# Kernel optimization log

Measured on AMD Instinct MI355X. Metric: run time of the kernel, lower is better.

Reference implementation:

```python
import jax, jax.numpy as jnp
import numpy as np

B, C, Q, E = 32, 1024, 64, 256  # batch, max_context_len, max_question_len, embedding_size
FE = 4 * E                      # final_encoding_size (self_attention=False)


def setup_inputs() -> dict:
    key = jax.random.key(0)
    ks = jax.random.split(key, 7)
    return {
        "context": jax.random.normal(ks[0], (B, C, E), dtype=jnp.float32),
        "question": jax.random.normal(ks[1], (B, Q, E), dtype=jnp.float32),
        "context_mask": jnp.ones((B, C), dtype=jnp.float32),
        "w_question": jax.random.normal(ks[2], (E,), dtype=jnp.float32),
        "w_context": jax.random.normal(ks[3], (E,), dtype=jnp.float32),
        "w_multiple": jax.random.normal(ks[4], (E,), dtype=jnp.float32),
        "final_W": jax.random.normal(ks[5], (FE, FE), dtype=jnp.float32) * (1.0 / np.sqrt(FE)),
        "final_b": jnp.zeros((FE,), dtype=jnp.float32),
    }


def reference(context, question, context_mask, w_question, w_context, w_multiple, final_W, final_b):
    # Trilinear similarity: s[b,c,q] = <w_q, q_q> + <w_c, c_c> + <w_m, c_c * q_q>
    q_weighted = question @ w_question                 # (B, Q)
    ctx_weighted = context @ w_context                 # (B, C)
    # (question.unsqueeze(1) * context.unsqueeze(2)) @ w_multiple, computed
    # without materializing the (B, C, Q, E) intermediate:
    mult = jnp.einsum('bce,bqe->bcq', context * w_multiple, question)  # (B, C, Q)
    similarity = ctx_weighted[:, :, None] + q_weighted[:, None, :] + mult  # (B, C, Q)

    # Context-to-query attention (softmax over question dim)
    c2q_att = jnp.einsum('bcq,bqe->bce', jax.nn.softmax(similarity, axis=2), question)

    # Query-to-context attention (softmax over context dim of row-max scores)
    q2c_weights = jax.nn.softmax(jnp.max(similarity, axis=2), axis=1)   # (B, C)
    q2c_att = jnp.einsum('bc,bce->be', q2c_weights, context)            # (B, E)

    attended = jnp.concatenate(
        [context, c2q_att, context * c2q_att, context * q2c_att[:, None, :]],
        axis=2)                                                          # (B, C, 4E)

    # MaskedLinear: affine map, output rows zeroed where context_mask == 0
    out = (attended @ final_W.T + final_b) * context_mask[:, :, None]    # (B, C, 4E)
    return out
```

## Files before the change

### kernel.cpp

```cpp
#include <hip/hip_runtime.h>

#define BB 32
#define CC 1024
#define QQ 64
#define EE 256
#define FE 1024
#define MM (BB*CC)

typedef __bf16 bf16_t;
typedef bf16_t bf16x8 __attribute__((ext_vector_type(8)));
typedef float f32x4 __attribute__((ext_vector_type(4)));

__device__ __forceinline__ unsigned short f2bf(float f) {
  unsigned u = __float_as_uint(f);
  u += 0x7fffu + ((u >> 16) & 1u);
  return (unsigned short)(u >> 16);
}
__device__ __forceinline__ float bf2f(unsigned short u) {
  return __uint_as_float(((unsigned)u) << 16);
}

__device__ __forceinline__ void gload_lds16(const void* g, void* l) {
  __builtin_amdgcn_global_load_lds(
      (const __attribute__((address_space(1))) unsigned int*)g,
      (__attribute__((address_space(3))) unsigned int*)l, 16, 0, 0);
}

__global__ void k_prep(const float* __restrict__ question, const float* __restrict__ w_question,
                       const float* __restrict__ w_multiple, float* __restrict__ qm,
                       float* __restrict__ qw,
                       const float* __restrict__ W, unsigned short* __restrict__ Wb) {
  int bx = blockIdx.x;
  if (bx < 512) {
    int gid = bx * 256 + threadIdx.x;
    int row = gid >> 6;
    int lane = gid & 63;
    const float4 q = *(const float4*)(question + (size_t)row * EE + lane * 4);
    const float4 wm = *(const float4*)(w_multiple + lane * 4);
    const float4 wq = *(const float4*)(w_question + lane * 4);
    float4 r; r.x = q.x*wm.x; r.y = q.y*wm.y; r.z = q.z*wm.z; r.w = q.w*wm.w;
    *(float4*)(qm + (size_t)row * EE + lane * 4) = r;
    float d = q.x*wq.x + q.y*wq.y + q.z*wq.z + q.w*wq.w;
    d += __shfl_xor(d, 1);  d += __shfl_xor(d, 2);  d += __shfl_xor(d, 4);
    d += __shfl_xor(d, 8);  d += __shfl_xor(d, 16); d += __shfl_xor(d, 32);
    if (lane == 0) qw[row] = d;
  } else {
    int i = ((bx - 512) * 256 + threadIdx.x) * 4;
    float4 v = *(const float4*)(W + i);
    ushort4 o; o.x = f2bf(v.x); o.y = f2bf(v.y); o.z = f2bf(v.z); o.w = f2bf(v.w);
    *(ushort4*)(Wb + i) = o;
  }
}

#define DOT4(acc, A, Bv) acc += A.x*Bv.x + A.y*Bv.y + A.z*Bv.z + A.w*Bv.w

__launch_bounds__(256)
__global__ void k_sim(const float* __restrict__ ctx, const float* __restrict__ qm,
                      const float* __restrict__ qw_g, const float* __restrict__ w_context,
                      float* __restrict__ P, float* __restrict__ rowmax,
                      unsigned short* __restrict__ att) {
  __shared__ float qml[QQ][260];
  __shared__ float ck[64][36];
  __shared__ float cwl[64];
  __shared__ float qwl[QQ];
  const int tid = threadIdx.x;
  const int b = blockIdx.y;
  const int c0 = blockIdx.x * 64;
  const int tx = tid & 15, ty = tid >> 4;

  const float* qmb = qm + (size_t)b * (QQ * EE);
  for (int idx = tid * 4; idx < QQ * EE; idx += 1024) {
    float4 v = *(const float4*)(qmb + idx);
    *(float4*)&qml[idx >> 8][idx & 255] = v;
  }
  if (tid < QQ) qwl[tid] = qw_g[b * QQ + tid];

  const int cr = tid >> 3, er = (tid & 7) * 4;
  const float* crow0 = ctx + ((size_t)(b * CC + c0 + cr)) * EE;
  const float* crow1 = crow0 + 32 * EE;
  unsigned short* arow0 = att + ((size_t)(b * CC + c0 + cr)) * FE;
  unsigned short* arow1 = arow0 + (size_t)32 * FE;
  float s[4][4] = {{0.f}};
  float cp0 = 0.f, cp1 = 0.f;

  for (int eo = 0; eo < EE; eo += 32) {
    float4 cv0 = *(const float4*)(crow0 + eo + er);
    float4 cv1 = *(const float4*)(crow1 + eo + er);
    float4 wc = *(const float4*)(w_context + eo + er);
    cp0 += cv0.x*wc.x + cv0.y*wc.y + cv0.z*wc.z + cv0.w*wc.w;
    cp1 += cv1.x*wc.x + cv1.y*wc.y + cv1.z*wc.z + cv1.w*wc.w;
    ushort4 u0, u1;
    u0.x = f2bf(cv0.x); u0.y = f2bf(cv0.y); u0.z = f2bf(cv0.z); u0.w = f2bf(cv0.w);
    u1.x = f2bf(cv1.x); u1.y = f2bf(cv1.y); u1.z = f2bf(cv1.z); u1.w = f2bf(cv1.w);
    *(ushort4*)(arow0 + eo + er) = u0;
    *(ushort4*)(arow1 + eo + er) = u1;
    __syncthreads();
    *(float4*)&ck[cr][er] = cv0;
    *(float4*)&ck[cr + 32][er] = cv1;
    __syncthreads();
#pragma unroll
    for (int ee = 0; ee < 32; ee += 4) {
      float4 a0 = *(const float4*)&ck[ty +  0][ee];
      float4 a1 = *(const float4*)&ck[ty + 16][ee];
      float4 a2 = *(const float4*)&ck[ty + 32][ee];
      float4 a3 = *(const float4*)&ck[ty + 48][ee];
      float4 b0 = *(const float4*)&qml[tx +  0][eo + ee];
      float4 b1 = *(const float4*)&qml[tx + 16][eo + ee];
      float4 b2 = *(const float4*)&qml[tx + 32][eo + ee];
      float4 b3 = *(const float4*)&qml[tx + 48][eo + ee];
      DOT4(s[0][0], a0, b0); DOT4(s[0][1], a0, b1); DOT4(s[0][2], a0, b2); DOT4(s[0][3], a0, b3);
      DOT4(s[1][0], a1, b0); DOT4(s[1][1], a1, b1); DOT4(s[1][2], a1, b2); DOT4(s[1][3], a1, b3);
      DOT4(s[2][0], a2, b0); DOT4(s[2][1], a2, b1); DOT4(s[2][2], a2, b2); DOT4(s[2][3], a2, b3);
      DOT4(s[3][0], a3, b0); DOT4(s[3][1], a3, b1); DOT4(s[3][2], a3, b2); DOT4(s[3][3], a3, b3);
    }
  }
  cp0 += __shfl_xor(cp0, 1); cp0 += __shfl_xor(cp0, 2); cp0 += __shfl_xor(cp0, 4);
  cp1 += __shfl_xor(cp1, 1); cp1 += __shfl_xor(cp1, 2); cp1 += __shfl_xor(cp1, 4);
  if ((tid & 7) == 0) { cwl[cr] = cp0; cwl[cr + 32] = cp1; }
  __syncthreads();

#pragma unroll
  for (int i = 0; i < 4; ++i) {
    int c = ty + 16 * i;
    float cw = cwl[c];
    float f[4], mx = -1e30f;
#pragma unroll
    for (int j = 0; j < 4; ++j) {
      f[j] = s[i][j] + cw + qwl[tx + 16 * j];
      mx = fmaxf(mx, f[j]);
    }
    mx = fmaxf(mx, __shfl_xor(mx, 1));
    mx = fmaxf(mx, __shfl_xor(mx, 2));
    mx = fmaxf(mx, __shfl_xor(mx, 4));
    mx = fmaxf(mx, __shfl_xor(mx, 8));
    float sum = 0.f;
#pragma unroll
    for (int j = 0; j < 4; ++j) { f[j] = expf(f[j] - mx); sum += f[j]; }
    sum += __shfl_xor(sum, 1);
    sum += __shfl_xor(sum, 2);
    sum += __shfl_xor(sum, 4);
    sum += __shfl_xor(sum, 8);
    float inv = 1.f / sum;
    if (tx == 0) rowmax[(size_t)b * CC + c0 + c] = mx;
    size_t prow = ((size_t)(b * CC + c0 + c)) * QQ;
#pragma unroll
    for (int j = 0; j < 4; ++j) P[prow + tx + 16 * j] = f[j] * inv;
  }
}

__global__ void k_q2c_softmax(const float* __restrict__ rowmax, float* __restrict__ q2cw) {
  int b = blockIdx.x, tid = threadIdx.x;
  __shared__ float rbuf[4], sbuf[4];
  float4 v = *(const float4*)(rowmax + (size_t)b * CC + tid * 4);
  float m = fmaxf(fmaxf(v.x, v.y), fmaxf(v.z, v.w));
  for (int off = 1; off < 64; off <<= 1) m = fmaxf(m, __shfl_xor(m, off));
  int wv = tid >> 6;
  if ((tid & 63) == 0) rbuf[wv] = m;
  __syncthreads();
  m = fmaxf(fmaxf(rbuf[0], rbuf[1]), fmaxf(rbuf[2], rbuf[3]));
  float e0 = expf(v.x - m), e1 = expf(v.y - m), e2 = expf(v.z - m), e3 = expf(v.w - m);
  float sum = e0 + e1 + e2 + e3;
  for (int off = 1; off < 64; off <<= 1) sum += __shfl_xor(sum, off);
  if ((tid & 63) == 0) sbuf[wv] = sum;
  __syncthreads();
  sum = sbuf[0] + sbuf[1] + sbuf[2] + sbuf[3];
  float inv = 1.f / sum;
  float4 o; o.x = e0 * inv; o.y = e1 * inv; o.z = e2 * inv; o.w = e3 * inv;
  *(float4*)(q2cw + (size_t)b * CC + tid * 4) = o;
}

__global__ void k_q2c_part(const unsigned short* __restrict__ att, const float* __restrict__ w,
                           float* __restrict__ part) {
  int b = blockIdx.y, ch = blockIdx.x;
  int e = threadIdx.x;
  const unsigned short* base = att + ((size_t)(b * CC + ch * 128)) * FE + e;
  const float* wp = w + b * CC + ch * 128;
  float acc = 0.f;
#pragma unroll 4
  for (int c = 0; c < 128; ++c) acc += wp[c] * bf2f(base[(size_t)c * FE]);
  part[(b * 8 + ch) * EE + e] = acc;
}

__global__ void k_q2c_sum(const float* __restrict__ part, float* __restrict__ q2catt) {
  int b = blockIdx.x, e = threadIdx.x;
  float a = 0.f;
#pragma unroll
  for (int ch = 0; ch < 8; ++ch) a += part[(b * 8 + ch) * EE + e];
  q2catt[b * EE + e] = a;
}

__launch_bounds__(256)
__global__ void k_pv(const float* __restrict__ P, const float* __restrict__ question,
                     const float* __restrict__ q2catt, unsigned short* __restrict__ attended) {
  __shared__ float PT[QQ][65];
  __shared__ float ql[QQ][68];
  const int tid = threadIdx.x;
  const int b = blockIdx.y, c0 = blockIdx.x * 64;
  const int tx = tid & 15, ty = tid >> 4;

  {
    int q4 = (tid & 15) * 4, cb = tid >> 4;
#pragma unroll
    for (int r = 0; r < 4; ++r) {
      int c = cb + 16 * r;
      float4 v = *(const float4*)(P + ((size_t)(b * CC + c0 + c)) * QQ + q4);
      PT[q4 + 0][c] = v.x; PT[q4 + 1][c] = v.y; PT[q4 + 2][c] = v.z; PT[q4 + 3][c] = v.w;
    }
  }
  const float* qb = question + (size_t)b * (QQ * EE);
  const float* g2 = q2catt + b * EE;

  for (int ep = 0; ep < EE; ep += 64) {
    __syncthreads();
    {
      int q = tid >> 2, e16 = (tid & 3) * 16;
      const float* src = qb + (size_t)q * EE + ep + e16;
      float4 v0 = *(const float4*)(src);
      float4 v1 = *(const float4*)(src + 4);
      float4 v2 = *(const float4*)(src + 8);
      float4 v3 = *(const float4*)(src + 12);
      *(float4*)&ql[q][e16]      = v0;
      *(float4*)&ql[q][e16 + 4]  = v1;
      *(float4*)&ql[q][e16 + 8]  = v2;
      *(float4*)&ql[q][e16 + 12] = v3;
    }
    __syncthreads();
    float s[4][4] = {{0.f}};
#pragma unroll 8
    for (int q = 0; q < QQ; ++q) {
      float a0 = PT[q][ty];
      float a1 = PT[q][ty + 16];
      float a2 = PT[q][ty + 32];
      float a3 = PT[q][ty + 48];
      float4 bv = *(const float4*)&ql[q][tx * 4];
      s[0][0] += a0 * bv.x; s[0][1] += a0 * bv.y; s[0][2] += a0 * bv.z; s[0][3] += a0 * bv.w;
      s[1][0] += a1 * bv.x; s[1][1] += a1 * bv.y; s[1][2] += a1 * bv.z; s[1][3] += a1 * bv.w;
      s[2][0] += a2 * bv.x; s[2][1] += a2 * bv.y; s[2][2] += a2 * bv.z; s[2][3] += a2 * bv.w;
      s[3][0] += a3 * bv.x; s[3][1] += a3 * bv.y; s[3][2] += a3 * bv.z; s[3][3] += a3 * bv.w;
    }
    float4 gv = *(const float4*)(g2 + ep + tx * 4);
#pragma unroll
    for (int i = 0; i < 4; ++i) {
      int c = ty + 16 * i;
      size_t row = (size_t)(b * CC + c0 + c);
      unsigned short* arow = attended + row * (size_t)FE;
      ushort4 cu = *(const ushort4*)(arow + 0 * EE + ep + tx * 4);
      float cx = bf2f(cu.x), cy = bf2f(cu.y), cz = bf2f(cu.z), cw = bf2f(cu.w);
      ushort4 s1, s2, s3;
      s1.x = f2bf(s[i][0]);        s1.y = f2bf(s[i][1]);        s1.z = f2bf(s[i][2]);        s1.w = f2bf(s[i][3]);
      s2.x = f2bf(cx * s[i][0]);   s2.y = f2bf(cy * s[i][1]);   s2.z = f2bf(cz * s[i][2]);   s2.w = f2bf(cw * s[i][3]);
      s3.x = f2bf(cx * gv.x);      s3.y = f2bf(cy * gv.y);      s3.z = f2bf(cz * gv.z);      s3.w = f2bf(cw * gv.w);
      *(ushort4*)(arow + 1 * EE + ep + tx * 4) = s1;
      *(ushort4*)(arow + 2 * EE + ep + tx * 4) = s2;
      *(ushort4*)(arow + 3 * EE + ep + tx * 4) = s3;
    }
  }
}

__launch_bounds__(512, 2)
__global__ void k_gemm(const unsigned short* __restrict__ A, const unsigned short* __restrict__ Bw,
                       const float* __restrict__ bias, const float* __restrict__ mask,
                       float* __restrict__ out) {
  __shared__ bf16_t As[2][2][128][64];
  __shared__ bf16_t Bs[2][2][128][64];
  const int tid = threadIdx.x;
  const int lane = tid & 63;
  const int wave = tid >> 6;
  const int wr = wave >> 2;
  const int wc = wave & 3;
  const int bh = wc >> 1;

  const int bid = blockIdx.x;
  const int wg = (bid & 7) * 64 + (bid >> 3);
  const int brow = (wg >> 2) * 256;
  const int bcol = (wg & 3) * 256;

  const int r = lane & 15, kg4 = lane >> 4;
  const int rx = r & 7;

  const int srow = tid >> 3;
  const int sg = (tid & 7) ^ (srow & 7);
  const unsigned short* gAb = A  + (size_t)(brow + srow) * FE + sg * 8;
  const unsigned short* gBb = Bw + (size_t)(bcol + srow) * FE + sg * 8;
  bf16_t* ldsAb = &As[0][0][srow][(tid & 7) * 8];
  bf16_t* ldsBb = &Bs[0][0][srow][(tid & 7) * 8];

  f32x4 acc[8][4] = {};
  bf16x8 faA[4][2], faB[4][2], fbA[2][2], fbB[2][2];

#define BARX __builtin_amdgcn_s_barrier()
#define VMW4 asm volatile("s_waitcnt vmcnt(4)" ::: "memory")
#define VMW0 asm volatile("s_waitcnt vmcnt(0)" ::: "memory")

#define ST_A(SLOT, H, KOFF) do {                                              \
    const unsigned short* s_ = gAb + (size_t)((H) * 128) * FE + (KOFF);       \
    bf16_t* d_ = ldsAb + ((SLOT) * 2 + (H)) * (128 * 64);                     \
    gload_lds16(s_, d_);                                                      \
    gload_lds16(s_ + (size_t)64 * FE, d_ + 64 * 64);                          \
  } while (0)
#define ST_B(SLOT, H, KOFF) do {                                              \
    const unsigned short* s_ = gBb + (size_t)((H) * 128) * FE + (KOFF);       \
    bf16_t* d_ = ldsBb + ((SLOT) * 2 + (H)) * (128 * 64);                     \
    gload_lds16(s_, d_);                                                      \
    gload_lds16(s_ + (size_t)64 * FE, d_ + 64 * 64);                          \
  } while (0)

#define RD_FA(DST, SLOT, MB) do {                                             \
    _Pragma("unroll") for (int mm = 0; mm < 4; ++mm) {                        \
      const int row_ = ((MB) + mm) * 16 + r;                                  \
      _Pragma("unroll") for (int ks = 0; ks < 2; ++ks)                        \
        DST[mm][ks] = *(const bf16x8*)&As[SLOT][wr][row_][((ks * 4 + kg4) ^ rx) * 8]; \
    } } while (0)
#define RD_FB(DST, SLOT, NB) do {                                             \
    _Pragma("unroll") for (int nn = 0; nn < 2; ++nn) {                        \
      const int row_ = (wc & 1) * 64 + ((NB) + nn) * 16 + r;                  \
      _Pragma("unroll") for (int ks = 0; ks < 2; ++ks)                        \
        DST[nn][ks] = *(const bf16x8*)&Bs[SLOT][bh][row_][((ks * 4 + kg4) ^ rx) * 8]; \
    } } while (0)

#define MFMA16(FA, FB, MB, NB) do {                                           \
    __builtin_amdgcn_s_setprio(1);                                            \
    _Pragma("unroll") for (int ks = 0; ks < 2; ++ks)                          \
    _Pragma("unroll") for (int mm = 0; mm < 4; ++mm)                          \
    _Pragma("unroll") for (int nn = 0; nn < 2; ++nn)                          \
      acc[(MB) + mm][(NB) + nn] = __builtin_amdgcn_mfma_f32_16x16x32_bf16(    \
          FA[mm][ks], FB[nn][ks], acc[(MB) + mm][(NB) + nn], 0, 0, 0);        \
    __builtin_amdgcn_s_setprio(0);                                            \
  } while (0)

  ST_B(0, 0, 0);  ST_B(0, 1, 0);  ST_A(0, 0, 0);  ST_A(0, 1, 0);
  ST_B(1, 0, 64); ST_B(1, 1, 64);
  VMW4;
  BARX;

#pragma unroll 1
  for (int i = 0; i < 8; ++i) {
    const int kT1 = (2 * i + 1) * 64;
    const int kT2 = (2 * i + 2) * 64;
    const int kT3 = (2 * i + 3) * 64;
    const bool more = (i < 7);

    RD_FA(faA, 0, 0); RD_FB(fbA, 0, 0);
    ST_A(1, 0, kT1);
    BARX; MFMA16(faA, fbA, 0, 0); BARX;
    RD_FB(fbB, 0, 2);
    ST_A(1, 1, kT1);
    BARX; MFMA16(faA, fbB, 0, 2); BARX;
    RD_FA(faB, 0, 4);
    if (more) ST_B(0, 0, kT2);
    BARX; MFMA16(faB, fbA, 4, 0); BARX;
    if (more) { ST_B(0, 1, kT2); VMW4; } else { VMW0; }
    BARX; MFMA16(faB, fbB, 4, 2); BARX;

    RD_FA(faA, 1, 0); RD_FB(fbA, 1, 0);
    if (more) ST_A(0, 0, kT2);
    BARX; MFMA16(faA, fbA, 0, 0); BARX;
    RD_FB(fbB, 1, 2);
    if (more) ST_A(0, 1, kT2);
    BARX; MFMA16(faA, fbB, 0, 2); BARX;
    RD_FA(faB, 1, 4);
    if (more) ST_B(1, 0, kT3);
    BARX; MFMA16(faB, fbA, 4, 0); BARX;
    if (more) { ST_B(1, 1, kT3); VMW4; }
    BARX; MFMA16(faB, fbB, 4, 2); BARX;
  }
#undef ST_A
#undef ST_B
#undef RD_FA
#undef RD_FB
#undef MFMA16

#pragma unroll
  for (int m = 0; m < 8; ++m) {
#pragma unroll
    for (int n = 0; n < 4; ++n) {
#pragma unroll
      for (int reg = 0; reg < 4; ++reg) {
        int row = brow + wr * 128 + m * 16 + kg4 * 4 + reg;
        int col = bcol + wc * 64 + n * 16 + r;
        out[(size_t)row * FE + col] = (acc[m][n][reg] + bias[col]) * mask[row];
      }
    }
  }
}

extern "C" void kernel_launch(void* const* d_in, const int* in_sizes, int n_in,
                              void* d_out, int out_size, void* d_ws, size_t ws_size,
                              hipStream_t stream) {
  const float* ctx  = (const float*)d_in[0];
  const float* ques = (const float*)d_in[1];
  const float* mask = (const float*)d_in[2];
  const float* w_q  = (const float*)d_in[3];
  const float* w_c  = (const float*)d_in[4];
  const float* w_m  = (const float*)d_in[5];
  const float* fW   = (const float*)d_in[6];
  const float* fb   = (const float*)d_in[7];
  float* out = (float*)d_out;

  char* ws = (char*)d_ws;
  float* qm     = (float*)(ws);
  float* qw     = (float*)(ws + 8388608);
  float* rowmax = (float*)(ws + 8396800);
  float* q2cw   = (float*)(ws + 8527872);
  float* part   = (float*)(ws + 8658944);
  float* q2catt = (float*)(ws + 8921088);
  float* P      = (float*)(ws + 8953856);
  unsigned short* attended = (unsigned short*)(ws + 17342464);
  unsigned short* Wb       = (unsigned short*)(ws + 84451328);

  k_prep<<<1536, 256, 0, stream>>>(ques, w_q, w_m, qm, qw, fW, Wb);
  k_sim<<<dim3(16, 32), 256, 0, stream>>>(ctx, qm, qw, w_c, P, rowmax, attended);
  k_q2c_softmax<<<32, 256, 0, stream>>>(rowmax, q2cw);
  k_q2c_part<<<dim3(8, 32), 256, 0, stream>>>(attended, q2cw, part);
  k_q2c_sum<<<32, 256, 0, stream>>>(part, q2catt);
  k_pv<<<dim3(16, 32), 256, 0, stream>>>(P, ques, q2catt, attended);
  k_gemm<<<512, 512, 0, stream>>>(attended, Wb, fb, mask, out);
}
```

Measured before the change: 184.2 us.

## Fuse similarity softmax with P·V and split out q2c product kernel

The softmax probabilities are now kept in shared memory as bf16 and multiplied with the question inside the similarity kernel, which removes the fp32 P round-trip through global memory and the separate k_pv kernel. The w_multiple scaling moves from a precomputed qm buffer to an in-register multiply on the context tile, and the question is staged in two halves to fit shared memory. A small elementwise kernel now writes the context*q2c block. In exchange, P is rounded to bf16 before the P·V product, and the fused kernel uses more shared memory, which may lower occupancy.

```diff
diff --git a/kernel.cpp b/kernel.cpp
--- a/kernel.cpp
+++ b/kernel.cpp
@@ -10,6 +10,7 @@
 typedef __bf16 bf16_t;
 typedef bf16_t bf16x8 __attribute__((ext_vector_type(8)));
 typedef float f32x4 __attribute__((ext_vector_type(4)));
+typedef unsigned short u16x8 __attribute__((ext_vector_type(8)));
 
 __device__ __forceinline__ unsigned short f2bf(float f) {
   unsigned u = __float_as_uint(f);
@@ -27,7 +28,6 @@
 }
 
 __global__ void k_prep(const float* __restrict__ question, const float* __restrict__ w_question,
-                       const float* __restrict__ w_multiple, float* __restrict__ qm,
                        float* __restrict__ qw,
                        const float* __restrict__ W, unsigned short* __restrict__ Wb) {
   int bx = blockIdx.x;
@@ -36,10 +36,7 @@
     int row = gid >> 6;
     int lane = gid & 63;
     const float4 q = *(const float4*)(question + (size_t)row * EE + lane * 4);
-    const float4 wm = *(const float4*)(w_multiple + lane * 4);
     const float4 wq = *(const float4*)(w_question + lane * 4);
-    float4 r; r.x = q.x*wm.x; r.y = q.y*wm.y; r.z = q.z*wm.z; r.w = q.w*wm.w;
-    *(float4*)(qm + (size_t)row * EE + lane * 4) = r;
     float d = q.x*wq.x + q.y*wq.y + q.z*wq.z + q.w*wq.w;
     d += __shfl_xor(d, 1);  d += __shfl_xor(d, 2);  d += __shfl_xor(d, 4);
     d += __shfl_xor(d, 8);  d += __shfl_xor(d, 16); d += __shfl_xor(d, 32);
@@ -55,12 +52,13 @@
 #define DOT4(acc, A, Bv) acc += A.x*Bv.x + A.y*Bv.y + A.z*Bv.z + A.w*Bv.w
 
 __launch_bounds__(256)
-__global__ void k_sim(const float* __restrict__ ctx, const float* __restrict__ qm,
-                      const float* __restrict__ qw_g, const float* __restrict__ w_context,
-                      float* __restrict__ P, float* __restrict__ rowmax,
-                      unsigned short* __restrict__ att) {
-  __shared__ float qml[QQ][260];
+__global__ void k_simpv(const float* __restrict__ ctx, const float* __restrict__ question,
+                        const float* __restrict__ qw_g, const float* __restrict__ w_context,
+                        const float* __restrict__ w_multiple,
+                        float* __restrict__ rowmax, unsigned short* __restrict__ att) {
+  __shared__ float qbuf[QQ * 132];
   __shared__ float ck[64][36];
+  __shared__ unsigned short Pl[QQ][68];
   __shared__ float cwl[64];
   __shared__ float qwl[QQ];
   const int tid = threadIdx.x;
@@ -68,11 +66,7 @@
   const int c0 = blockIdx.x * 64;
   const int tx = tid & 15, ty = tid >> 4;
 
-  const float* qmb = qm + (size_t)b * (QQ * EE);
-  for (int idx = tid * 4; idx < QQ * EE; idx += 1024) {
-    float4 v = *(const float4*)(qmb + idx);
-    *(float4*)&qml[idx >> 8][idx & 255] = v;
-  }
+  const float* qb = question + (size_t)b * (QQ * EE);
   if (tid < QQ) qwl[tid] = qw_g[b * QQ + tid];
 
   const int cr = tid >> 3, er = (tid & 7) * 4;
@@ -83,35 +77,47 @@
   float s[4][4] = {{0.f}};
   float cp0 = 0.f, cp1 = 0.f;
 
-  for (int eo = 0; eo < EE; eo += 32) {
-    float4 cv0 = *(const float4*)(crow0 + eo + er);
-    float4 cv1 = *(const float4*)(crow1 + eo + er);
-    float4 wc = *(const float4*)(w_context + eo + er);
-    cp0 += cv0.x*wc.x + cv0.y*wc.y + cv0.z*wc.z + cv0.w*wc.w;
-    cp1 += cv1.x*wc.x + cv1.y*wc.y + cv1.z*wc.z + cv1.w*wc.w;
-    ushort4 u0, u1;
-    u0.x = f2bf(cv0.x); u0.y = f2bf(cv0.y); u0.z = f2bf(cv0.z); u0.w = f2bf(cv0.w);
-    u1.x = f2bf(cv1.x); u1.y = f2bf(cv1.y); u1.z = f2bf(cv1.z); u1.w = f2bf(cv1.w);
-    *(ushort4*)(arow0 + eo + er) = u0;
-    *(ushort4*)(arow1 + eo + er) = u1;
-    __syncthreads();
-    *(float4*)&ck[cr][er] = cv0;
-    *(float4*)&ck[cr + 32][er] = cv1;
-    __syncthreads();
-#pragma unroll
-    for (int ee = 0; ee < 32; ee += 4) {
-      float4 a0 = *(const float4*)&ck[ty +  0][ee];
-      float4 a1 = *(const float4*)&ck[ty + 16][ee];
-      float4 a2 = *(const float4*)&ck[ty + 32][ee];
-      float4 a3 = *(const float4*)&ck[ty + 48][ee];
-      float4 b0 = *(const float4*)&qml[tx +  0][eo + ee];
-      float4 b1 = *(const float4*)&qml[tx + 16][eo + ee];
-      float4 b2 = *(const float4*)&qml[tx + 32][eo + ee];
-      float4 b3 = *(const float4*)&qml[tx + 48][eo + ee];
-      DOT4(s[0][0], a0, b0); DOT4(s[0][1], a0, b1); DOT4(s[0][2], a0, b2); DOT4(s[0][3], a0, b3);
-      DOT4(s[1][0], a1, b0); DOT4(s[1][1], a1, b1); DOT4(s[1][2], a1, b2); DOT4(s[1][3], a1, b3);
-      DOT4(s[2][0], a2, b0); DOT4(s[2][1], a2, b1); DOT4(s[2][2], a2, b2); DOT4(s[2][3], a2, b3);
-      DOT4(s[3][0], a3, b0); DOT4(s[3][1], a3, b1); DOT4(s[3][2], a3, b2); DOT4(s[3][3], a3, b3);
+  for (int h = 0; h < 2; ++h) {
+    if (h) __syncthreads();
+    for (int idx = tid * 4; idx < QQ * 128; idx += 1024) {
+      int row = idx >> 7, col = idx & 127;
+      *(float4*)&qbuf[row * 132 + col] = *(const float4*)(qb + (size_t)row * EE + h * 128 + col);
+    }
+    for (int eo2 = 0; eo2 < 128; eo2 += 32) {
+      const int eo = h * 128 + eo2;
+      float4 cv0 = *(const float4*)(crow0 + eo + er);
+      float4 cv1 = *(const float4*)(crow1 + eo + er);
+      float4 wc = *(const float4*)(w_context + eo + er);
+      float4 wm = *(const float4*)(w_multiple + eo + er);
+      cp0 += cv0.x*wc.x + cv0.y*wc.y + cv0.z*wc.z + cv0.w*wc.w;
+      cp1 += cv1.x*wc.x + cv1.y*wc.y + cv1.z*wc.z + cv1.w*wc.w;
+      ushort4 u0, u1;
+      u0.x = f2bf(cv0.x); u0.y = f2bf(cv0.y); u0.z = f2bf(cv0.z); u0.w = f2bf(cv0.w);
+      u1.x = f2bf(cv1.x); u1.y = f2bf(cv1.y); u1.z = f2bf(cv1.z); u1.w = f2bf(cv1.w);
+      *(ushort4*)(arow0 + eo + er) = u0;
+      *(ushort4*)(arow1 + eo + er) = u1;
+      __syncthreads();
+      float4 m0, m1;
+      m0.x = cv0.x*wm.x; m0.y = cv0.y*wm.y; m0.z = cv0.z*wm.z; m0.w = cv0.w*wm.w;
+      m1.x = cv1.x*wm.x; m1.y = cv1.y*wm.y; m1.z = cv1.z*wm.z; m1.w = cv1.w*wm.w;
+      *(float4*)&ck[cr][er] = m0;
+      *(float4*)&ck[cr + 32][er] = m1;
+      __syncthreads();
+#pragma unroll
+      for (int ee = 0; ee < 32; ee += 4) {
+        float4 a0 = *(const float4*)&ck[ty +  0][ee];
+        float4 a1 = *(const float4*)&ck[ty + 16][ee];
+        float4 a2 = *(const float4*)&ck[ty + 32][ee];
+        float4 a3 = *(const float4*)&ck[ty + 48][ee];
+        float4 b0 = *(const float4*)&qbuf[(tx +  0) * 132 + eo2 + ee];
+        float4 b1 = *(const float4*)&qbuf[(tx + 16) * 132 + eo2 + ee];
+        float4 b2 = *(const float4*)&qbuf[(tx + 32) * 132 + eo2 + ee];
+        float4 b3 = *(const float4*)&qbuf[(tx + 48) * 132 + eo2 + ee];
+        DOT4(s[0][0], a0, b0); DOT4(s[0][1], a0, b1); DOT4(s[0][2], a0, b2); DOT4(s[0][3], a0, b3);
+        DOT4(s[1][0], a1, b0); DOT4(s[1][1], a1, b1); DOT4(s[1][2], a1, b2); DOT4(s[1][3], a1, b3);
+        DOT4(s[2][0], a2, b0); DOT4(s[2][1], a2, b1); DOT4(s[2][2], a2, b2); DOT4(s[2][3], a2, b3);
+        DOT4(s[3][0], a3, b0); DOT4(s[3][1], a3, b1); DOT4(s[3][2], a3, b2); DOT4(s[3][3], a3, b3);
+      }
     }
   }
   cp0 += __shfl_xor(cp0, 1); cp0 += __shfl_xor(cp0, 2); cp0 += __shfl_xor(cp0, 4);
@@ -142,9 +148,48 @@
     sum += __shfl_xor(sum, 8);
     float inv = 1.f / sum;
     if (tx == 0) rowmax[(size_t)b * CC + c0 + c] = mx;
-    size_t prow = ((size_t)(b * CC + c0 + c)) * QQ;
-#pragma unroll
-    for (int j = 0; j < 4; ++j) P[prow + tx + 16 * j] = f[j] * inv;
+#pragma unroll
+    for (int j = 0; j < 4; ++j) Pl[tx + 16 * j][c] = f2bf(f[j] * inv);
+  }
+  __syncthreads();
+
+  for (int ep = 0; ep < EE; ep += 64) {
+    if (ep) __syncthreads();
+    {
+      int q = tid >> 2, e16 = (tid & 3) * 16;
+      const float* src = qb + (size_t)q * EE + ep + e16;
+      *(float4*)&qbuf[q * 68 + e16 +  0] = *(const float4*)(src);
+      *(float4*)&qbuf[q * 68 + e16 +  4] = *(const float4*)(src + 4);
+      *(float4*)&qbuf[q * 68 + e16 +  8] = *(const float4*)(src + 8);
+      *(float4*)&qbuf[q * 68 + e16 + 12] = *(const float4*)(src + 12);
+    }
+    __syncthreads();
+    float s2[4][4] = {{0.f}};
+#pragma unroll 8
+    for (int q = 0; q < QQ; ++q) {
+      float a0 = bf2f(Pl[q][ty +  0]);
+      float a1 = bf2f(Pl[q][ty + 16]);
+      float a2 = bf2f(Pl[q][ty + 32]);
+      float a3 = bf2f(Pl[q][ty + 48]);
+      float4 bv = *(const float4*)&qbuf[q * 68 + tx * 4];
+      s2[0][0] += a0 * bv.x; s2[0][1] += a0 * bv.y; s2[0][2] += a0 * bv.z; s2[0][3] += a0 * bv.w;
+      s2[1][0] += a1 * bv.x; s2[1][1] += a1 * bv.y; s2[1][2] += a1 * bv.z; s2[1][3] += a1 * bv.w;
+      s2[2][0] += a2 * bv.x; s2[2][1] += a2 * bv.y; s2[2][2] += a2 * bv.z; s2[2][3] += a2 * bv.w;
+      s2[3][0] += a3 * bv.x; s2[3][1] += a3 * bv.y; s2[3][2] += a3 * bv.z; s2[3][3] += a3 * bv.w;
+    }
+#pragma unroll
+    for (int i = 0; i < 4; ++i) {
+      int c = ty + 16 * i;
+      size_t row = (size_t)(b * CC + c0 + c);
+      unsigned short* arow = att + row * (size_t)FE;
+      ushort4 cu = *(const ushort4*)(arow + ep + tx * 4);
+      float cx = bf2f(cu.x), cy = bf2f(cu.y), cz = bf2f(cu.z), cw = bf2f(cu.w);
+      ushort4 o1, o2;
+      o1.x = f2bf(s2[i][0]);       o1.y = f2bf(s2[i][1]);       o1.z = f2bf(s2[i][2]);       o1.w = f2bf(s2[i][3]);
+      o2.x = f2bf(cx * s2[i][0]);  o2.y = f2bf(cy * s2[i][1]);  o2.z = f2bf(cz * s2[i][2]);  o2.w = f2bf(cw * s2[i][3]);
+      *(ushort4*)(arow + 1 * EE + ep + tx * 4) = o1;
+      *(ushort4*)(arow + 2 * EE + ep + tx * 4) = o2;
+    }
   }
 }
 
@@ -189,72 +234,21 @@
   q2catt[b * EE + e] = a;
 }
 
-__launch_bounds__(256)
-__global__ void k_pv(const float* __restrict__ P, const float* __restrict__ question,
-                     const float* __restrict__ q2catt, unsigned short* __restrict__ attended) {
-  __shared__ float PT[QQ][65];
-  __shared__ float ql[QQ][68];
-  const int tid = threadIdx.x;
-  const int b = blockIdx.y, c0 = blockIdx.x * 64;
-  const int tx = tid & 15, ty = tid >> 4;
-
-  {
-    int q4 = (tid & 15) * 4, cb = tid >> 4;
-#pragma unroll
-    for (int r = 0; r < 4; ++r) {
-      int c = cb + 16 * r;
-      float4 v = *(const float4*)(P + ((size_t)(b * CC + c0 + c)) * QQ + q4);
-      PT[q4 + 0][c] = v.x; PT[q4 + 1][c] = v.y; PT[q4 + 2][c] = v.z; PT[q4 + 3][c] = v.w;
-    }
-  }
-  const float* qb = question + (size_t)b * (QQ * EE);
-  const float* g2 = q2catt + b * EE;
-
-  for (int ep = 0; ep < EE; ep += 64) {
-    __syncthreads();
-    {
-      int q = tid >> 2, e16 = (tid & 3) * 16;
-      const float* src = qb + (size_t)q * EE + ep + e16;
-      float4 v0 = *(const float4*)(src);
-      float4 v1 = *(const float4*)(src + 4);
-      float4 v2 = *(const float4*)(src + 8);
-      float4 v3 = *(const float4*)(src + 12);
-      *(float4*)&ql[q][e16]      = v0;
-      *(float4*)&ql[q][e16 + 4]  = v1;
-      *(float4*)&ql[q][e16 + 8]  = v2;
-      *(float4*)&ql[q][e16 + 12] = v3;
-    }
-    __syncthreads();
-    float s[4][4] = {{0.f}};
-#pragma unroll 8
-    for (int q = 0; q < QQ; ++q) {
-      float a0 = PT[q][ty];
-      float a1 = PT[q][ty + 16];
-      float a2 = PT[q][ty + 32];
-      float a3 = PT[q][ty + 48];
-      float4 bv = *(const float4*)&ql[q][tx * 4];
-      s[0][0] += a0 * bv.x; s[0][1] += a0 * bv.y; s[0][2] += a0 * bv.z; s[0][3] += a0 * bv.w;
-      s[1][0] += a1 * bv.x; s[1][1] += a1 * bv.y; s[1][2] += a1 * bv.z; s[1][3] += a1 * bv.w;
-      s[2][0] += a2 * bv.x; s[2][1] += a2 * bv.y; s[2][2] += a2 * bv.z; s[2][3] += a2 * bv.w;
-      s[3][0] += a3 * bv.x; s[3][1] += a3 * bv.y; s[3][2] += a3 * bv.z; s[3][3] += a3 * bv.w;
-    }
-    float4 gv = *(const float4*)(g2 + ep + tx * 4);
-#pragma unroll
-    for (int i = 0; i < 4; ++i) {
-      int c = ty + 16 * i;
-      size_t row = (size_t)(b * CC + c0 + c);
-      unsigned short* arow = attended + row * (size_t)FE;
-      ushort4 cu = *(const ushort4*)(arow + 0 * EE + ep + tx * 4);
-      float cx = bf2f(cu.x), cy = bf2f(cu.y), cz = bf2f(cu.z), cw = bf2f(cu.w);
-      ushort4 s1, s2, s3;
-      s1.x = f2bf(s[i][0]);        s1.y = f2bf(s[i][1]);        s1.z = f2bf(s[i][2]);        s1.w = f2bf(s[i][3]);
-      s2.x = f2bf(cx * s[i][0]);   s2.y = f2bf(cy * s[i][1]);   s2.z = f2bf(cz * s[i][2]);   s2.w = f2bf(cw * s[i][3]);
-      s3.x = f2bf(cx * gv.x);      s3.y = f2bf(cy * gv.y);      s3.z = f2bf(cz * gv.z);      s3.w = f2bf(cw * gv.w);
-      *(ushort4*)(arow + 1 * EE + ep + tx * 4) = s1;
-      *(ushort4*)(arow + 2 * EE + ep + tx * 4) = s2;
-      *(ushort4*)(arow + 3 * EE + ep + tx * 4) = s3;
-    }
-  }
+__global__ void k_att3(const unsigned short* __restrict__ att_ro, const float* __restrict__ q2catt,
+                       unsigned short* __restrict__ att_wr) {
+  int unit = blockIdx.x * 256 + threadIdx.x;
+  int row = unit >> 5;
+  int e8 = (unit & 31) * 8;
+  int b = row >> 10;
+  u16x8 c = *(const u16x8*)(att_ro + (size_t)row * FE + e8);
+  float4 g0 = *(const float4*)(q2catt + b * EE + e8);
+  float4 g1 = *(const float4*)(q2catt + b * EE + e8 + 4);
+  u16x8 o;
+  o[0] = f2bf(bf2f(c[0]) * g0.x); o[1] = f2bf(bf2f(c[1]) * g0.y);
+  o[2] = f2bf(bf2f(c[2]) * g0.z); o[3] = f2bf(bf2f(c[3]) * g0.w);
+  o[4] = f2bf(bf2f(c[4]) * g1.x); o[5] = f2bf(bf2f(c[5]) * g1.y);
+  o[6] = f2bf(bf2f(c[6]) * g1.z); o[7] = f2bf(bf2f(c[7]) * g1.w);
+  *(u16x8*)(att_wr + (size_t)row * FE + 3 * EE + e8) = o;
 }
 
 __launch_bounds__(512, 2)
@@ -398,21 +392,19 @@
   float* out = (float*)d_out;
 
   char* ws = (char*)d_ws;
-  float* qm     = (float*)(ws);
-  float* qw     = (float*)(ws + 8388608);
-  float* rowmax = (float*)(ws + 8396800);
-  float* q2cw   = (float*)(ws + 8527872);
-  float* part   = (float*)(ws + 8658944);
-  float* q2catt = (float*)(ws + 8921088);
-  float* P      = (float*)(ws + 8953856);
-  unsigned short* attended = (unsigned short*)(ws + 17342464);
-  unsigned short* Wb       = (unsigned short*)(ws + 84451328);
-
-  k_prep<<<1536, 256, 0, stream>>>(ques, w_q, w_m, qm, qw, fW, Wb);
-  k_sim<<<dim3(16, 32), 256, 0, stream>>>(ctx, qm, qw, w_c, P, rowmax, attended);
+  float* qw     = (float*)(ws);
+  float* rowmax = (float*)(ws + 8192);
+  float* q2cw   = (float*)(ws + 139264);
+  float* part   = (float*)(ws + 270336);
+  float* q2catt = (float*)(ws + 532480);
+  unsigned short* attended = (unsigned short*)(ws + 1048576);
+  unsigned short* Wb       = (unsigned short*)(ws + 68157440);
+
+  k_prep<<<1536, 256, 0, stream>>>(ques, w_q, qw, fW, Wb);
+  k_simpv<<<dim3(16, 32), 256, 0, stream>>>(ctx, ques, qw, w_c, w_m, rowmax, attended);
   k_q2c_softmax<<<32, 256, 0, stream>>>(rowmax, q2cw);
   k_q2c_part<<<dim3(8, 32), 256, 0, stream>>>(attended, q2cw, part);
   k_q2c_sum<<<32, 256, 0, stream>>>(part, q2catt);
-  k_pv<<<dim3(16, 32), 256, 0, stream>>>(P, ques, q2catt, attended);
+  k_att3<<<4096, 256, 0, stream>>>(attended, q2catt, attended);
   k_gemm<<<512, 512, 0, stream>>>(attended, Wb, fb, mask, out);
 }
```

Result: faster. 160.7 us (-12.8%).
